# Performance work log

Hardware: AMD Instinct MI355X
Metric: run time of the kernel (lower is better)

The kernel has to match this reference:

```python
import jax, jax.numpy as jnp
import numpy as np

B, NB, D, T, K = 8, 3, 512, 2048, 1024


def setup_inputs() -> dict:
    key = jax.random.key(0)
    k1, k2 = jax.random.split(key)
    x = jax.random.normal(k1, (B, NB, D, T), dtype=jnp.float32)
    codebook = jax.random.normal(k2, (NB, K, D), dtype=jnp.float32)
    return {"x": x, "codebook": codebook}


def reference(x, codebook):
    """Band vector quantization forward.

    x:        [B, NB, D, T]  (channels-first frames, one chunk per band)
    codebook: [NB, K, D]     (one Euclidean codebook per band)
    Returns (quantized [B,NB,D,T], codes [B,NB,T] int32, commit_loss scalar).
    """
    xt = jnp.swapaxes(x, -1, -2)  # [B, NB, T, D]
    x2 = jnp.sum(xt * xt, axis=-1, keepdims=True)          # [B, NB, T, 1]
    e2 = jnp.sum(codebook * codebook, axis=-1)              # [NB, K]
    xe = jnp.einsum('bntd,nkd->bntk', xt, codebook)         # [B, NB, T, K]
    dist = x2 - 2.0 * xe + e2[None, :, None, :]
    codes = jnp.argmin(dist, axis=-1)                       # [B, NB, T]
    # gather nearest codewords per band
    band_idx = jnp.arange(NB).reshape(1, NB, 1)
    q = codebook[band_idx, codes]                           # [B, NB, T, D]
    # commitment loss: MSE(sg(quantized), x), mean over bands
    commit_loss = jnp.mean((jax.lax.stop_gradient(q) - xt) ** 2)
    # straight-through estimator
    q_st = xt + jax.lax.stop_gradient(q - xt)
    quantized = jnp.swapaxes(q_st, -1, -2)                  # [B, NB, D, T]
    return quantized, codes, commit_loss
```

## Files before the change

kernel.cpp:

```cpp
#include <hip/hip_runtime.h>


#define B_ 8
#define NB_ 3
#define D_ 512
#define T_ 2048
#define K_ 1024
#define BN_ (B_*NB_)
#define ROWS_ (BN_*T_)
#define Q_ELEMS_ ((size_t)BN_*D_*T_)
#define MARGIN_ 0.02f
#define FLAGCAP_ 8192
#define RESCAN_BLOCKS_ 128

typedef __attribute__((ext_vector_type(4))) float f32x4;
typedef __attribute__((ext_vector_type(8))) short bf16x8;
typedef __attribute__((ext_vector_type(4))) unsigned int u32x4;

__device__ inline unsigned short f2bf(float f) {
    unsigned u = __builtin_bit_cast(unsigned, f);
    unsigned r = (u + 0x7FFFu + ((u >> 16) & 1u)) >> 16;
    return (unsigned short)r;
}
__device__ inline float bf2f(unsigned short h) {
    unsigned u = ((unsigned)h) << 16;
    return __builtin_bit_cast(float, u);
}
__device__ inline void gld16(const void* g, void* l) {
    __builtin_amdgcn_global_load_lds(
        (const __attribute__((address_space(1))) unsigned int*)g,
        (__attribute__((address_space(3))) unsigned int*)l, 16, 0, 0);
}

__global__ void zero_ws(float* __restrict__ x2g, float* __restrict__ lossp,
                        int* __restrict__ flag_cnt) {
    int i = blockIdx.x * 256 + threadIdx.x;
    if (i < ROWS_) x2g[i] = 0.f;
    if (i == 0) { *lossp = 0.f; *flag_cnt = 0; }
}

__global__ __launch_bounds__(256) void convert_e(
    const float* __restrict__ cb,
    unsigned short* __restrict__ Eh, unsigned short* __restrict__ El,
    float* __restrict__ e2) {
    int row = blockIdx.x * 4 + (threadIdx.x >> 6);
    int lane = threadIdx.x & 63;
    const float* p = cb + (size_t)row * D_ + lane * 8;
    float v[8];
#pragma unroll
    for (int e = 0; e < 8; ++e) v[e] = p[e];
    double sum = 0.0;
#pragma unroll
    for (int e = 0; e < 8; ++e) sum += (double)v[e] * (double)v[e];
    unsigned int uh[4], ul[4];
#pragma unroll
    for (int q = 0; q < 4; ++q) {
        unsigned short h0 = f2bf(v[2*q]), h1 = f2bf(v[2*q+1]);
        float l0 = v[2*q] - bf2f(h0), l1 = v[2*q+1] - bf2f(h1);
        uh[q] = (unsigned)h0 | ((unsigned)h1 << 16);
        ul[q] = (unsigned)f2bf(l0) | ((unsigned)f2bf(l1) << 16);
    }
    size_t pos = (size_t)row * 1024 + lane * 16;
    *(u32x4*)((char*)Eh + pos) = u32x4{uh[0], uh[1], uh[2], uh[3]};
    *(u32x4*)((char*)El + pos) = u32x4{ul[0], ul[1], ul[2], ul[3]};
    for (int off = 32; off > 0; off >>= 1) sum += __shfl_down(sum, off, 64);
    if (lane == 0) e2[row] = (float)sum;
}

__global__ __launch_bounds__(256) void convert_x(
    const float* __restrict__ x,
    unsigned short* __restrict__ Xh, unsigned short* __restrict__ Xl,
    float* __restrict__ x2g) {
    int t0 = blockIdx.x * 64;
    int sl = blockIdx.y;
    int bn = blockIdx.z;
    int d0 = sl * 64;
    int tid = threadIdx.x;
    __shared__ float tile[64][65];
#pragma unroll
    for (int i = 0; i < 16; ++i) {
        int idx = tid + 256 * i;
        int dd = idx >> 6, tt = idx & 63;
        tile[dd][tt] = x[((size_t)bn * D_ + d0 + dd) * T_ + t0 + tt];
    }
    __syncthreads();
    int tt = tid >> 2, cp = tid & 3;
    size_t rowbyte = ((size_t)bn * T_ + t0 + tt) * 1024 + (size_t)sl * 128;
    float s2 = 0.f;
#pragma unroll
    for (int cc = 0; cc < 2; ++cc) {
        int c = cp * 2 + cc;
        unsigned int uh[4], ul[4];
#pragma unroll
        for (int q = 0; q < 4; ++q) {
            float v0 = tile[c * 8 + 2*q][tt], v1 = tile[c * 8 + 2*q + 1][tt];
            s2 += v0 * v0 + v1 * v1;
            unsigned short h0 = f2bf(v0), h1 = f2bf(v1);
            float l0 = v0 - bf2f(h0), l1 = v1 - bf2f(h1);
            uh[q] = (unsigned)h0 | ((unsigned)h1 << 16);
            ul[q] = (unsigned)f2bf(l0) | ((unsigned)f2bf(l1) << 16);
        }
        size_t pos = rowbyte + c * 16;
        *(u32x4*)((char*)Xh + pos) = u32x4{uh[0], uh[1], uh[2], uh[3]};
        *(u32x4*)((char*)Xl + pos) = u32x4{ul[0], ul[1], ul[2], ul[3]};
    }
    s2 += __shfl_xor(s2, 1, 64);
    s2 += __shfl_xor(s2, 2, 64);
    if (cp == 0) atomicAdd(&x2g[(size_t)bn * T_ + t0 + tt], s2);
}

__global__ __launch_bounds__(512, 2) void vq_gemm(
    const unsigned short* __restrict__ Xh, const unsigned short* __restrict__ Xl,
    const unsigned short* __restrict__ Eh, const unsigned short* __restrict__ El,
    const float* __restrict__ e2,
    float* __restrict__ pm1, float* __restrict__ pm2, int* __restrict__ pi1) {

    __shared__ char lds[131072];
    int tid = threadIdx.x;
    int lane = tid & 63, wid = tid >> 6;
    int bx = blockIdx.x, by = blockIdx.y, bn = blockIdx.z;
    int band = bn % NB_;
    int wm = wid >> 2, wn = wid & 3;
    int rl = lane & 15, cl = lane >> 4;

    int smat = wid >> 1;
    const char* srcm = (smat == 0) ? (const char*)Xh : (smat == 1) ? (const char*)Xl
                     : (smat == 2) ? (const char*)Eh : (const char*)El;
    size_t rowbase = (smat < 2) ? ((size_t)bn * T_ + (size_t)bx * 256)
                                : ((size_t)band * K_ + (size_t)by * 256);
    const char* lane_src = srcm + (rowbase + (wid & 1) * 128 + (lane >> 2)) * 1024
                         + (((lane & 3) ^ ((lane >> 3) & 3)) * 16);
    const int dstoff = (wid >> 1) * 16384 + (wid & 1) * 8192;
    const int chunkoff = ((cl ^ ((rl >> 1) & 3)) * 16);

    f32x4 acc[8][4];
#pragma unroll
    for (int m = 0; m < 8; ++m)
#pragma unroll
        for (int n = 0; n < 4; ++n) acc[m][n] = f32x4{0.f, 0.f, 0.f, 0.f};

    {
        char* dp = lds + dstoff;
#pragma unroll
        for (int q = 0; q < 8; ++q) gld16(lane_src + (size_t)q * 16384, dp + q * 1024);
    }

    for (int s = 0; s < 16; ++s) {
        if (s < 15) {
            const char* sp = lane_src + (size_t)(s + 1) * 64;
            char* dp = lds + ((s + 1) & 1) * 65536 + dstoff;
#pragma unroll
            for (int q = 0; q < 8; ++q) gld16(sp + (size_t)q * 16384, dp + q * 1024);
            __builtin_amdgcn_sched_barrier(0);
            asm volatile("s_waitcnt vmcnt(8)" ::: "memory");
        } else {
            __builtin_amdgcn_sched_barrier(0);
            asm volatile("s_waitcnt vmcnt(0)" ::: "memory");
        }
        __builtin_amdgcn_sched_barrier(0);
        __builtin_amdgcn_s_barrier();

        const char* base = lds + (s & 1) * 65536;
        bf16x8 bh[4], bl[4];
#pragma unroll
        for (int n = 0; n < 4; ++n) {
            int boff = (wn * 64 + n * 16 + rl) * 64 + chunkoff;
            bh[n] = *(const bf16x8*)(base + 32768 + boff);
            bl[n] = *(const bf16x8*)(base + 49152 + boff);
        }
        __builtin_amdgcn_s_setprio(1);
#pragma unroll
        for (int m = 0; m < 8; ++m) {
            int aoff = (wm * 128 + m * 16 + rl) * 64 + chunkoff;
            bf16x8 ah = *(const bf16x8*)(base + aoff);
            bf16x8 al = *(const bf16x8*)(base + 16384 + aoff);
#pragma unroll
            for (int n = 0; n < 4; ++n) {
                acc[m][n] = __builtin_amdgcn_mfma_f32_16x16x32_bf16(ah, bh[n], acc[m][n], 0, 0, 0);
                acc[m][n] = __builtin_amdgcn_mfma_f32_16x16x32_bf16(ah, bl[n], acc[m][n], 0, 0, 0);
                acc[m][n] = __builtin_amdgcn_mfma_f32_16x16x32_bf16(al, bh[n], acc[m][n], 0, 0, 0);
            }
        }
        __builtin_amdgcn_s_setprio(0);
        asm volatile("s_waitcnt lgkmcnt(0)" ::: "memory");
        __builtin_amdgcn_sched_barrier(0);
        __builtin_amdgcn_s_barrier();
    }

    int kb = by * 256 + wn * 64 + rl;
    float ev[4];
#pragma unroll
    for (int n = 0; n < 4; ++n) ev[n] = e2[band * K_ + kb + n * 16];

    float tm1[32], tm2[32];
    int ti[32];
#pragma unroll
    for (int m = 0; m < 8; ++m)
#pragma unroll
        for (int r = 0; r < 4; ++r) {
            int id = m * 4 + r;
            float a1 = 3.4e38f, a2 = 3.4e38f; int i1 = 0;
#pragma unroll
            for (int n = 0; n < 4; ++n) {
                float v = ev[n] - 2.0f * acc[m][n][r];
                int k = kb + n * 16;
                if (v < a1) { a2 = a1; a1 = v; i1 = k; }
                else if (v < a2) a2 = v;
            }
            tm1[id] = a1; tm2[id] = a2; ti[id] = i1;
        }
#pragma unroll
    for (int id = 0; id < 32; ++id) {
#pragma unroll
        for (int st = 1; st < 16; st <<= 1) {
            float om1 = __shfl_xor(tm1[id], st, 64);
            float om2 = __shfl_xor(tm2[id], st, 64);
            int   oi  = __shfl_xor(ti[id],  st, 64);
            if (om1 < tm1[id] || (om1 == tm1[id] && oi < ti[id])) {
                tm2[id] = fminf(tm1[id], om2); tm1[id] = om1; ti[id] = oi;
            } else {
                tm2[id] = fminf(tm2[id], om1);
            }
        }
    }
    float* mm1 = (float*)lds;
    float* mm2 = (float*)(lds + 4096);
    int*   mi  = (int*)(lds + 8192);
    __syncthreads();
    if (rl == 0) {
#pragma unroll
        for (int m = 0; m < 8; ++m)
#pragma unroll
            for (int r = 0; r < 4; ++r) {
                int row = wm * 128 + m * 16 + cl * 4 + r;
                mm1[wn * 256 + row] = tm1[m * 4 + r];
                mm2[wn * 256 + row] = tm2[m * 4 + r];
                mi [wn * 256 + row] = ti [m * 4 + r];
            }
    }
    __syncthreads();
    if (tid < 256) {
        float m1 = mm1[tid], m2 = mm2[tid]; int i1 = mi[tid];
#pragma unroll
        for (int j = 1; j < 4; ++j) {
            float b1 = mm1[j * 256 + tid], b2 = mm2[j * 256 + tid];
            int   bi = mi[j * 256 + tid];
            if (b1 < m1 || (b1 == m1 && bi < i1)) { m2 = fminf(m1, b2); m1 = b1; i1 = bi; }
            else m2 = fminf(m2, b1);
        }
        size_t gr = (size_t)bn * T_ + (size_t)bx * 256 + tid;
        pm1[gr * 4 + by] = m1; pm2[gr * 4 + by] = m2; pi1[gr * 4 + by] = i1;
    }
}

__global__ __launch_bounds__(256) void finalize_kernel(
    const float* __restrict__ pm1, const float* __restrict__ pm2,
    const int* __restrict__ pi1, const float* __restrict__ x2g,
    float* __restrict__ outc, float* __restrict__ lossp,
    int* __restrict__ flag_cnt, int* __restrict__ flag_list) {
    int row = blockIdx.x * 256 + threadIdx.x;
    size_t r4 = (size_t)row * 4;
    float m1 = pm1[r4], m2 = pm2[r4]; int i1 = pi1[r4];
#pragma unroll
    for (int j = 1; j < 4; ++j) {
        float b1 = pm1[r4 + j], b2 = pm2[r4 + j]; int bi = pi1[r4 + j];
        if (b1 < m1) { m2 = fminf(m1, b2); m1 = b1; i1 = bi; }
        else m2 = fminf(m2, b1);
    }
    float lrow = x2g[row] + m1;
    if (m2 - m1 < MARGIN_) {
        int slot = atomicAdd(flag_cnt, 1);
        if (slot < FLAGCAP_) { flag_list[slot] = row; lrow = 0.f; }
        else outc[row] = (float)i1;
    } else {
        outc[row] = (float)i1;
    }
    for (int off = 32; off > 0; off >>= 1) lrow += __shfl_down(lrow, off, 64);
    __shared__ float ws4[4];
    if ((threadIdx.x & 63) == 0) ws4[threadIdx.x >> 6] = lrow;
    __syncthreads();
    if (threadIdx.x == 0)
        atomicAdd(lossp, (ws4[0] + ws4[1] + ws4[2] + ws4[3]) * (1.0f / (float)Q_ELEMS_));
}

__global__ __launch_bounds__(256) void rescan_kernel(
    const float* __restrict__ x, const float* __restrict__ cb,
    const int* __restrict__ flag_cnt, const int* __restrict__ flag_list,
    float* __restrict__ outc, float* __restrict__ lossp) {
    int tid = threadIdx.x;
    int cnt = *flag_cnt; if (cnt > FLAGCAP_) cnt = FLAGCAP_;
    __shared__ float xsh[D_];
    __shared__ double rv[256];
    __shared__ int    ri[256];
    for (int i = blockIdx.x; i < cnt; i += RESCAN_BLOCKS_) {
        int row = flag_list[i];
        int bn = row / T_, t = row % T_;
        int band = bn % NB_;
        __syncthreads();
        for (int d = tid; d < D_; d += 256)
            xsh[d] = x[((size_t)bn * D_ + d) * T_ + t];
        __syncthreads();
        double best = 1e300; int bi = K_;
        for (int k = tid; k < K_; k += 256) {
            const float* cr = cb + ((size_t)band * K_ + k) * D_;
            double s = 0.0;
            for (int d = 0; d < D_; d += 4) {
                float4 c4 = *(const float4*)(cr + d);
                double e0 = (double)xsh[d]     - (double)c4.x;
                double e1 = (double)xsh[d + 1] - (double)c4.y;
                double e2v = (double)xsh[d + 2] - (double)c4.z;
                double e3 = (double)xsh[d + 3] - (double)c4.w;
                s += e0 * e0 + e1 * e1 + e2v * e2v + e3 * e3;
            }
            if (s < best) { best = s; bi = k; }
        }
        rv[tid] = best; ri[tid] = bi;
        __syncthreads();
        for (int s2 = 128; s2 > 0; s2 >>= 1) {
            if (tid < s2) {
                if (rv[tid + s2] < rv[tid] ||
                    (rv[tid + s2] == rv[tid] && ri[tid + s2] < ri[tid])) {
                    rv[tid] = rv[tid + s2]; ri[tid] = ri[tid + s2];
                }
            }
            __syncthreads();
        }
        if (tid == 0) {
            outc[row] = (float)ri[0];
            atomicAdd(lossp, (float)(rv[0] * (1.0 / (double)Q_ELEMS_)));
        }
    }
}

__global__ __launch_bounds__(256) void gather_out(
    const float* __restrict__ cb, const float* __restrict__ outc,
    float* __restrict__ outq) {
    int t0 = blockIdx.x * 64;
    int sl = blockIdx.y;
    int bn = blockIdx.z;
    int d0 = sl * 64;
    int band = bn % NB_;
    int tid = threadIdx.x;
    int wv = tid >> 6, ln = tid & 63;
    __shared__ float qsh[64][65];
    __shared__ int csh[64];
    if (tid < 64) csh[tid] = (int)outc[(size_t)bn * T_ + t0 + tid];
    __syncthreads();
    const float* cbb = cb + (size_t)band * K_ * D_ + d0;
#pragma unroll
    for (int j = 0; j < 16; ++j) {
        int r = wv * 16 + j;
        qsh[r][ln] = cbb[(size_t)csh[r] * D_ + ln];
    }
    __syncthreads();
#pragma unroll
    for (int j = 0; j < 16; ++j) {
        int dd = wv * 16 + j;
        outq[((size_t)bn * D_ + d0 + dd) * T_ + t0 + ln] = qsh[ln][dd];
    }
}

extern "C" void kernel_launch(void* const* d_in, const int* in_sizes, int n_in,
                              void* d_out, int out_size, void* d_ws, size_t ws_size,
                              hipStream_t stream) {
    (void)in_sizes; (void)n_in; (void)out_size; (void)ws_size;
    const float* x  = (const float*)d_in[0];
    const float* cb = (const float*)d_in[1];
    float* out = (float*)d_out;

    float* outq  = out;
    float* outc  = out + Q_ELEMS_;
    float* lossp = out + Q_ELEMS_ + ROWS_;

    unsigned short* Xh = (unsigned short*)d_out;
    unsigned short* Xl = Xh + Q_ELEMS_;

    char* ws = (char*)d_ws;
    unsigned short* Eh = (unsigned short*)ws;
    unsigned short* El = Eh + (size_t)NB_ * K_ * D_;
    float* e2  = (float*)(El + (size_t)NB_ * K_ * D_);
    float* x2g = e2 + NB_ * K_;
    float* pm1 = x2g + ROWS_;
    float* pm2 = pm1 + (size_t)ROWS_ * 4;
    int*   pi1 = (int*)(pm2 + (size_t)ROWS_ * 4);
    int*   flag_cnt  = pi1 + (size_t)ROWS_ * 4;
    int*   flag_list = flag_cnt + 1;

    zero_ws<<<dim3((ROWS_ + 255) / 256), dim3(256), 0, stream>>>(x2g, lossp, flag_cnt);
    convert_e<<<dim3(768), dim3(256), 0, stream>>>(cb, Eh, El, e2);
    convert_x<<<dim3(32, 8, 24), dim3(256), 0, stream>>>(x, Xh, Xl, x2g);
    vq_gemm<<<dim3(8, 4, 24), dim3(512), 0, stream>>>(Xh, Xl, Eh, El, e2, pm1, pm2, pi1);
    finalize_kernel<<<dim3(ROWS_ / 256), dim3(256), 0, stream>>>(
        pm1, pm2, pi1, x2g, outc, lossp, flag_cnt, flag_list);
    rescan_kernel<<<dim3(RESCAN_BLOCKS_), dim3(256), 0, stream>>>(
        x, cb, flag_cnt, flag_list, outc, lossp);
    gather_out<<<dim3(32, 8, 24), dim3(256), 0, stream>>>(cb, outc, outq);
}
```

Measured before the change: 308.1 us.

## Replace split-bf16 three-pass GEMM with single-pass fp16 GEMM and wider rescan margin

Drops the hi/lo bf16 split of x and the codebook and computes the distance GEMM with a single fp16 MFMA pass instead of three bf16 passes. This cuts MFMA work to a third, halves the converted-operand traffic and the LDS tile size, and raises the occupancy hint to 4 blocks. The lower precision is offset by widening the near-tie margin so that more rows are flagged for exact fp32 rescan, and rescan gets more blocks. The risk is that many more rows get flagged, possibly overflowing the flag capacity, and that the rescan kernel becomes the bottleneck.

```diff
diff --git a/kernel.cpp b/kernel.cpp
--- a/kernel.cpp
+++ b/kernel.cpp
@@ -9,22 +9,17 @@
 #define BN_ (B_*NB_)
 #define ROWS_ (BN_*T_)
 #define Q_ELEMS_ ((size_t)BN_*D_*T_)
-#define MARGIN_ 0.02f
+#define MARGIN_ 0.10f
 #define FLAGCAP_ 8192
-#define RESCAN_BLOCKS_ 128
+#define RESCAN_BLOCKS_ 256
 
 typedef __attribute__((ext_vector_type(4))) float f32x4;
-typedef __attribute__((ext_vector_type(8))) short bf16x8;
+typedef __attribute__((ext_vector_type(8))) _Float16 f16x8;
 typedef __attribute__((ext_vector_type(4))) unsigned int u32x4;
 
-__device__ inline unsigned short f2bf(float f) {
-    unsigned u = __builtin_bit_cast(unsigned, f);
-    unsigned r = (u + 0x7FFFu + ((u >> 16) & 1u)) >> 16;
-    return (unsigned short)r;
-}
-__device__ inline float bf2f(unsigned short h) {
-    unsigned u = ((unsigned)h) << 16;
-    return __builtin_bit_cast(float, u);
+__device__ inline unsigned short f2h(float f) {
+    _Float16 h = (_Float16)f;
+    return __builtin_bit_cast(unsigned short, h);
 }
 __device__ inline void gld16(const void* g, void* l) {
     __builtin_amdgcn_global_load_lds(
@@ -41,8 +36,7 @@
 
 __global__ __launch_bounds__(256) void convert_e(
     const float* __restrict__ cb,
-    unsigned short* __restrict__ Eh, unsigned short* __restrict__ El,
-    float* __restrict__ e2) {
+    unsigned short* __restrict__ Eh, float* __restrict__ e2) {
     int row = blockIdx.x * 4 + (threadIdx.x >> 6);
     int lane = threadIdx.x & 63;
     const float* p = cb + (size_t)row * D_ + lane * 8;
@@ -52,25 +46,19 @@
     double sum = 0.0;
 #pragma unroll
     for (int e = 0; e < 8; ++e) sum += (double)v[e] * (double)v[e];
-    unsigned int uh[4], ul[4];
-#pragma unroll
-    for (int q = 0; q < 4; ++q) {
-        unsigned short h0 = f2bf(v[2*q]), h1 = f2bf(v[2*q+1]);
-        float l0 = v[2*q] - bf2f(h0), l1 = v[2*q+1] - bf2f(h1);
-        uh[q] = (unsigned)h0 | ((unsigned)h1 << 16);
-        ul[q] = (unsigned)f2bf(l0) | ((unsigned)f2bf(l1) << 16);
-    }
-    size_t pos = (size_t)row * 1024 + lane * 16;
-    *(u32x4*)((char*)Eh + pos) = u32x4{uh[0], uh[1], uh[2], uh[3]};
-    *(u32x4*)((char*)El + pos) = u32x4{ul[0], ul[1], ul[2], ul[3]};
+    unsigned int uh[4];
+#pragma unroll
+    for (int q = 0; q < 4; ++q)
+        uh[q] = (unsigned)f2h(v[2*q]) | ((unsigned)f2h(v[2*q+1]) << 16);
+    *(u32x4*)((char*)Eh + (size_t)row * 1024 + lane * 16) =
+        u32x4{uh[0], uh[1], uh[2], uh[3]};
     for (int off = 32; off > 0; off >>= 1) sum += __shfl_down(sum, off, 64);
     if (lane == 0) e2[row] = (float)sum;
 }
 
 __global__ __launch_bounds__(256) void convert_x(
     const float* __restrict__ x,
-    unsigned short* __restrict__ Xh, unsigned short* __restrict__ Xl,
-    float* __restrict__ x2g) {
+    unsigned short* __restrict__ Xh, float* __restrict__ x2g) {
     int t0 = blockIdx.x * 64;
     int sl = blockIdx.y;
     int bn = blockIdx.z;
@@ -90,32 +78,26 @@
 #pragma unroll
     for (int cc = 0; cc < 2; ++cc) {
         int c = cp * 2 + cc;
-        unsigned int uh[4], ul[4];
+        unsigned int uh[4];
 #pragma unroll
         for (int q = 0; q < 4; ++q) {
             float v0 = tile[c * 8 + 2*q][tt], v1 = tile[c * 8 + 2*q + 1][tt];
             s2 += v0 * v0 + v1 * v1;
-            unsigned short h0 = f2bf(v0), h1 = f2bf(v1);
-            float l0 = v0 - bf2f(h0), l1 = v1 - bf2f(h1);
-            uh[q] = (unsigned)h0 | ((unsigned)h1 << 16);
-            ul[q] = (unsigned)f2bf(l0) | ((unsigned)f2bf(l1) << 16);
-        }
-        size_t pos = rowbyte + c * 16;
-        *(u32x4*)((char*)Xh + pos) = u32x4{uh[0], uh[1], uh[2], uh[3]};
-        *(u32x4*)((char*)Xl + pos) = u32x4{ul[0], ul[1], ul[2], ul[3]};
+            uh[q] = (unsigned)f2h(v0) | ((unsigned)f2h(v1) << 16);
+        }
+        *(u32x4*)((char*)Xh + rowbyte + c * 16) = u32x4{uh[0], uh[1], uh[2], uh[3]};
     }
     s2 += __shfl_xor(s2, 1, 64);
     s2 += __shfl_xor(s2, 2, 64);
     if (cp == 0) atomicAdd(&x2g[(size_t)bn * T_ + t0 + tt], s2);
 }
 
-__global__ __launch_bounds__(512, 2) void vq_gemm(
-    const unsigned short* __restrict__ Xh, const unsigned short* __restrict__ Xl,
-    const unsigned short* __restrict__ Eh, const unsigned short* __restrict__ El,
+__global__ __launch_bounds__(512, 4) void vq_gemm(
+    const unsigned short* __restrict__ Xh, const unsigned short* __restrict__ Eh,
     const float* __restrict__ e2,
     float* __restrict__ pm1, float* __restrict__ pm2, int* __restrict__ pi1) {
 
-    __shared__ char lds[131072];
+    __shared__ char lds[65536];
     int tid = threadIdx.x;
     int lane = tid & 63, wid = tid >> 6;
     int bx = blockIdx.x, by = blockIdx.y, bn = blockIdx.z;
@@ -123,14 +105,14 @@
     int wm = wid >> 2, wn = wid & 3;
     int rl = lane & 15, cl = lane >> 4;
 
-    int smat = wid >> 1;
-    const char* srcm = (smat == 0) ? (const char*)Xh : (smat == 1) ? (const char*)Xl
-                     : (smat == 2) ? (const char*)Eh : (const char*)El;
-    size_t rowbase = (smat < 2) ? ((size_t)bn * T_ + (size_t)bx * 256)
-                                : ((size_t)band * K_ + (size_t)by * 256);
-    const char* lane_src = srcm + (rowbase + (wid & 1) * 128 + (lane >> 2)) * 1024
+    int is_b = wid >> 2;
+    int wq = wid & 3;
+    const char* srcm = is_b ? (const char*)Eh : (const char*)Xh;
+    size_t rowbase = is_b ? ((size_t)band * K_ + (size_t)by * 256)
+                          : ((size_t)bn * T_ + (size_t)bx * 256);
+    const char* lane_src = srcm + (rowbase + wq * 64 + (lane >> 2)) * 1024
                          + (((lane & 3) ^ ((lane >> 3) & 3)) * 16);
-    const int dstoff = (wid >> 1) * 16384 + (wid & 1) * 8192;
+    const int dstoff = is_b * 16384 + wq * 4096;
     const int chunkoff = ((cl ^ ((rl >> 1) & 3)) * 16);
 
     f32x4 acc[8][4];
@@ -142,17 +124,17 @@
     {
         char* dp = lds + dstoff;
 #pragma unroll
-        for (int q = 0; q < 8; ++q) gld16(lane_src + (size_t)q * 16384, dp + q * 1024);
+        for (int q = 0; q < 4; ++q) gld16(lane_src + (size_t)q * 16384, dp + q * 1024);
     }
 
     for (int s = 0; s < 16; ++s) {
         if (s < 15) {
             const char* sp = lane_src + (size_t)(s + 1) * 64;
-            char* dp = lds + ((s + 1) & 1) * 65536 + dstoff;
-#pragma unroll
-            for (int q = 0; q < 8; ++q) gld16(sp + (size_t)q * 16384, dp + q * 1024);
+            char* dp = lds + ((s + 1) & 1) * 32768 + dstoff;
+#pragma unroll
+            for (int q = 0; q < 4; ++q) gld16(sp + (size_t)q * 16384, dp + q * 1024);
             __builtin_amdgcn_sched_barrier(0);
-            asm volatile("s_waitcnt vmcnt(8)" ::: "memory");
+            asm volatile("s_waitcnt vmcnt(4)" ::: "memory");
         } else {
             __builtin_amdgcn_sched_barrier(0);
             asm volatile("s_waitcnt vmcnt(0)" ::: "memory");
@@ -160,28 +142,18 @@
         __builtin_amdgcn_sched_barrier(0);
         __builtin_amdgcn_s_barrier();
 
-        const char* base = lds + (s & 1) * 65536;
-        bf16x8 bh[4], bl[4];
-#pragma unroll
-        for (int n = 0; n < 4; ++n) {
-            int boff = (wn * 64 + n * 16 + rl) * 64 + chunkoff;
-            bh[n] = *(const bf16x8*)(base + 32768 + boff);
-            bl[n] = *(const bf16x8*)(base + 49152 + boff);
-        }
-        __builtin_amdgcn_s_setprio(1);
+        const char* base = lds + (s & 1) * 32768;
+        f16x8 bh[4];
+#pragma unroll
+        for (int n = 0; n < 4; ++n)
+            bh[n] = *(const f16x8*)(base + 16384 + (wn * 64 + n * 16 + rl) * 64 + chunkoff);
 #pragma unroll
         for (int m = 0; m < 8; ++m) {
-            int aoff = (wm * 128 + m * 16 + rl) * 64 + chunkoff;
-            bf16x8 ah = *(const bf16x8*)(base + aoff);
-            bf16x8 al = *(const bf16x8*)(base + 16384 + aoff);
-#pragma unroll
-            for (int n = 0; n < 4; ++n) {
-                acc[m][n] = __builtin_amdgcn_mfma_f32_16x16x32_bf16(ah, bh[n], acc[m][n], 0, 0, 0);
-                acc[m][n] = __builtin_amdgcn_mfma_f32_16x16x32_bf16(ah, bl[n], acc[m][n], 0, 0, 0);
-                acc[m][n] = __builtin_amdgcn_mfma_f32_16x16x32_bf16(al, bh[n], acc[m][n], 0, 0, 0);
-            }
-        }
-        __builtin_amdgcn_s_setprio(0);
+            f16x8 ah = *(const f16x8*)(base + (wm * 128 + m * 16 + rl) * 64 + chunkoff);
+#pragma unroll
+            for (int n = 0; n < 4; ++n)
+                acc[m][n] = __builtin_amdgcn_mfma_f32_16x16x32_f16(ah, bh[n], acc[m][n], 0, 0, 0);
+        }
         asm volatile("s_waitcnt lgkmcnt(0)" ::: "memory");
         __builtin_amdgcn_sched_barrier(0);
         __builtin_amdgcn_s_barrier();
@@ -373,12 +345,10 @@
     float* lossp = out + Q_ELEMS_ + ROWS_;
 
     unsigned short* Xh = (unsigned short*)d_out;
-    unsigned short* Xl = Xh + Q_ELEMS_;
 
     char* ws = (char*)d_ws;
     unsigned short* Eh = (unsigned short*)ws;
-    unsigned short* El = Eh + (size_t)NB_ * K_ * D_;
-    float* e2  = (float*)(El + (size_t)NB_ * K_ * D_);
+    float* e2  = (float*)(Eh + (size_t)NB_ * K_ * D_);
     float* x2g = e2 + NB_ * K_;
     float* pm1 = x2g + ROWS_;
     float* pm2 = pm1 + (size_t)ROWS_ * 4;
@@ -387,9 +357,9 @@
     int*   flag_list = flag_cnt + 1;
 
     zero_ws<<<dim3((ROWS_ + 255) / 256), dim3(256), 0, stream>>>(x2g, lossp, flag_cnt);
-    convert_e<<<dim3(768), dim3(256), 0, stream>>>(cb, Eh, El, e2);
-    convert_x<<<dim3(32, 8, 24), dim3(256), 0, stream>>>(x, Xh, Xl, x2g);
-    vq_gemm<<<dim3(8, 4, 24), dim3(512), 0, stream>>>(Xh, Xl, Eh, El, e2, pm1, pm2, pi1);
+    convert_e<<<dim3(768), dim3(256), 0, stream>>>(cb, Eh, e2);
+    convert_x<<<dim3(32, 8, 24), dim3(256), 0, stream>>>(x, Xh, x2g);
+    vq_gemm<<<dim3(8, 4, 24), dim3(512), 0, stream>>>(Xh, Eh, e2, pm1, pm2, pi1);
     finalize_kernel<<<dim3(ROWS_ / 256), dim3(256), 0, stream>>>(
         pm1, pm2, pi1, x2g, outc, lossp, flag_cnt, flag_list);
     rescan_kernel<<<dim3(RESCAN_BLOCKS_), dim3(256), 0, stream>>>(
```

New measurement: 625.6 us. +103.0%, slower.
